# Kernel optimization log

Measured on AMD Instinct MI355X. Metric: run time of the kernel, lower is better.

Reference implementation:

```python
import jax, jax.numpy as jnp
import numpy as np

B, T, D = 1024, 256, 3
H, K, A = 128, 4, 2


def _xavier(key, shape):
    # xavier_uniform over the last two dims (per-expert [H, fan_in])
    fan_out, fan_in = shape[-2], shape[-1]
    lim = float(np.sqrt(6.0 / (fan_in + fan_out)))
    return jax.random.uniform(key, shape, minval=-lim, maxval=lim, dtype=jnp.float32)


def setup_inputs() -> dict:
    key = jax.random.key(0)
    ks = jax.random.split(key, 9)
    x = jax.random.uniform(ks[0], (B, T, D), dtype=jnp.float32)
    inp = {
        'x': x,
        'Wxr': _xavier(ks[1], (K, H, D)),
        'Wxz': _xavier(ks[2], (K, H, D)),
        'Wxn': _xavier(ks[3], (K, H, D)),
        'Whr': _xavier(ks[4], (K, H, H)),
        'Whz': _xavier(ks[5], (K, H, H)),
        'Whn': _xavier(ks[6], (K, H, H)),
        'bxr': jnp.zeros((K, H), jnp.float32),
        'bxz': jnp.zeros((K, H), jnp.float32),
        'bxn': jnp.zeros((K, H), jnp.float32),
        'brh': jnp.zeros((K, H), jnp.float32),
        'bzh': jnp.zeros((K, H), jnp.float32),
        'bnh': jnp.zeros((K, H), jnp.float32),
        'Wout': jax.random.normal(ks[7], (A, H), dtype=jnp.float32) / np.sqrt(H),
        'bout': jnp.zeros((A,), jnp.float32),
    }
    return inp


def _selector(x_t):
    # modes: 0:(a=1,r=0) 1:(a=2,r=0) 2:(a=1,r=1) 3:(a=2,r=1)
    a = jnp.argmax(x_t[:, :2], axis=-1)
    r = (x_t[:, 2] > 0.5).astype(jnp.int32)
    return jax.nn.one_hot(a + 2 * r, K, dtype=x_t.dtype)  # (B, K)


def reference(x, Wxr, Wxz, Wxn, Whr, Whz, Whn,
              bxr, bxz, bxn, brh, bzh, bnh, Wout, bout):
    def step(h, x_t):
        u = _selector(x_t)  # (B, K) one-hot
        # mixing is linear, so mix(W) @ v == mix(W @ v): compute per-expert
        # gate pre-activations then select/mix with u (avoids B*H*H temp).
        def aff_x(W, b):
            g = jnp.einsum('khd,bd->bkh', W, x_t)
            return jnp.einsum('bkh,bk->bh', g, u) + u @ b
        def aff_h(W, b):
            g = jnp.einsum('kij,bj->bki', W, h)
            return jnp.einsum('bki,bk->bi', g, u) + u @ b
        r_t = jax.nn.sigmoid(aff_x(Wxr, bxr) + aff_h(Whr, brh))
        z_t = jax.nn.sigmoid(aff_x(Wxz, bxz) + aff_h(Whz, bzh))
        n_t = jnp.tanh(aff_x(Wxn, bxn) + r_t * aff_h(Whn, bnh))
        h_new = (1.0 - z_t) * n_t + z_t * h
        logits_t = h_new @ Wout.T + bout  # (B, A)
        return h_new, logits_t

    h0 = jnp.zeros((x.shape[0], H), x.dtype)
    hT, logits_tbA = jax.lax.scan(step, h0, jnp.swapaxes(x, 0, 1))
    return jnp.swapaxes(logits_tbA, 0, 1), hT  # (B, T, A), (B, H)
```

## Files before the change

kernel.cpp:

```cpp
#include <hip/hip_runtime.h>

#define Bn 1024
#define Tn 256

typedef __attribute__((ext_vector_type(4))) float f32x4;
typedef __attribute__((ext_vector_type(2))) float f32x2;
typedef __attribute__((ext_vector_type(8))) short short8;

static __device__ __forceinline__ unsigned pack_bf16_2(float lo, float hi) {
    unsigned ul = __float_as_uint(lo), uh = __float_as_uint(hi);
    ul = (ul + 0x7fffu + ((ul >> 16) & 1u)) >> 16;
    uh = (uh + 0x7fffu + ((uh >> 16) & 1u)) >> 16;
    return (ul & 0xffffu) | (uh << 16);
}

static __device__ __forceinline__ unsigned short f2bf(float f) {
    unsigned u = __float_as_uint(f);
    return (unsigned short)((u + 0x7fffu + ((u >> 16) & 1u)) >> 16);
}

__launch_bounds__(512, 2)
__global__ void bandit_rnn(const float* __restrict__ x,
                           const float* __restrict__ Wxr, const float* __restrict__ Wxz, const float* __restrict__ Wxn,
                           const float* __restrict__ Whr, const float* __restrict__ Whz, const float* __restrict__ Whn,
                           const float* __restrict__ bxr, const float* __restrict__ bxz, const float* __restrict__ bxn,
                           const float* __restrict__ brh, const float* __restrict__ bzh, const float* __restrict__ bnh,
                           const float* __restrict__ Wout, const float* __restrict__ bout,
                           float* __restrict__ out) {
    __shared__ f32x4 comb0[512], comb1[512], comb2[512];
    __shared__ float combB[512];
    __shared__ __align__(16) unsigned short h16[2][4][136];
    __shared__ float WoutL[256];
    __shared__ float xs[2][4][3];
    __shared__ unsigned modesArr[Tn];
    __shared__ __align__(16) float spbuf[2][8][4][2];

    const int tid = threadIdx.x;
    const int w = tid >> 6;
    const int lane = tid & 63;
    const int r16 = lane & 15, q = lane >> 4;
    const int cb = blockIdx.x * 4;

    for (int p = tid; p < 2 * 4 * 136; p += 512) ((unsigned short*)h16)[p] = 0;
    {
        int p = tid;
        int k = p >> 7, i = p & 127;
        const float* wr = Wxr + (k * 128 + i) * 3;
        const float* wz = Wxz + (k * 128 + i) * 3;
        const float* wn = Wxn + (k * 128 + i) * 3;
        comb0[p] = (f32x4){wr[0], wr[1], wr[2], bxr[p] + brh[p]};
        comb1[p] = (f32x4){wz[0], wz[1], wz[2], bxz[p] + bzh[p]};
        comb2[p] = (f32x4){wn[0], wn[1], wn[2], bxn[p]};
        combB[p] = bnh[p];
    }
    if (tid < 256) WoutL[tid] = Wout[tid];
    const float b0 = bout[0], b1 = bout[1];

    if (tid < Tn) {
        const float* xp = x + (size_t)cb * (Tn * 3) + tid * 3;
        unsigned mword = 0;
#pragma unroll
        for (int c = 0; c < 4; ++c) {
            float x0 = xp[c * Tn * 3 + 0];
            float x1 = xp[c * Tn * 3 + 1];
            float x2 = xp[c * Tn * 3 + 2];
            unsigned mode = ((x1 > x0) ? 1u : 0u) + ((x2 > 0.5f) ? 2u : 0u);
            mword |= mode << (8 * c);
        }
        modesArr[tid] = mword;
    }
    if (tid < 12) {
        int c = tid / 3, j = tid % 3;
        xs[0][c][j] = x[(size_t)(cb + c) * (Tn * 3) + j];
    }

    short8 Afr[3][4][4];
    {
        const float* Wh[3] = {Whr, Whz, Whn};
#pragma unroll
        for (int g = 0; g < 3; ++g)
#pragma unroll
        for (int e = 0; e < 4; ++e)
#pragma unroll
        for (int kt = 0; kt < 4; ++kt) {
            const float* p = Wh[g] + (((e * 128) + (16 * w + r16)) * 128 + 32 * kt + 8 * q);
            float4 a0 = *(const float4*)p;
            float4 a1 = *(const float4*)(p + 4);
            union { short8 s; unsigned u[4]; } fr;
            fr.u[0] = pack_bf16_2(a0.x, a0.y);
            fr.u[1] = pack_bf16_2(a0.z, a0.w);
            fr.u[2] = pack_bf16_2(a1.x, a1.y);
            fr.u[3] = pack_bf16_2(a1.z, a1.w);
            Afr[g][e][kt] = fr.s;
        }
    }

    const int cc = r16 & 3;
    const bool jb0 = ((r16 >> 2) & 1) != 0;
    const bool jb1 = ((r16 >> 2) & 2) != 0;
    const int row = 16 * w + 4 * q + (r16 >> 2);
    float hpv = 0.f;
    __syncthreads();

#pragma unroll 1
    for (int t = 0; t < Tn; ++t) {
        const int tb = t & 1;
        if (t > 0 && tid < 8) {
            int c = tid >> 1, a = tid & 1;
            float s = a ? b1 : b0;
#pragma unroll
            for (int wv = 0; wv < 8; ++wv) s += spbuf[tb ^ 1][wv][c][a];
            out[((size_t)(cb + c) * Tn + (t - 1)) * 2 + a] = s;
        }
        float xpre = 0.f; int xc = 0, xj = 0;
        if (t + 1 < Tn && tid < 12) {
            xc = tid / 3; xj = tid % 3;
            xpre = x[(size_t)(cb + xc) * (Tn * 3) + (t + 1) * 3 + xj];
        }

        const unsigned m = modesArr[t];
        const unsigned pres = (1u << (m & 3)) | (1u << ((m >> 8) & 3)) |
                              (1u << ((m >> 16) & 3)) | (1u << ((m >> 24) & 3));
        const int mode_c = (m >> (8 * cc)) & 3;

        short8 Bf[4];
#pragma unroll
        for (int kt = 0; kt < 4; ++kt)
            Bf[kt] = *(const short8*)&h16[tb][cc][32 * kt + 8 * q];

        float selR = 0.f, selZ = 0.f, selN = 0.f;
#pragma unroll
        for (int e = 0; e < 4; ++e) {
            if (!(pres & (1u << e))) continue;
            f32x4 aR = (f32x4){0.f, 0.f, 0.f, 0.f};
            f32x4 aZ = (f32x4){0.f, 0.f, 0.f, 0.f};
            f32x4 aN = (f32x4){0.f, 0.f, 0.f, 0.f};
#pragma unroll
            for (int kt = 0; kt < 4; ++kt) {
                aR = __builtin_amdgcn_mfma_f32_16x16x32_bf16(Afr[0][e][kt], Bf[kt], aR, 0, 0, 0);
                aZ = __builtin_amdgcn_mfma_f32_16x16x32_bf16(Afr[1][e][kt], Bf[kt], aZ, 0, 0, 0);
                aN = __builtin_amdgcn_mfma_f32_16x16x32_bf16(Afr[2][e][kt], Bf[kt], aN, 0, 0, 0);
            }
            float vR = jb1 ? (jb0 ? aR[3] : aR[2]) : (jb0 ? aR[1] : aR[0]);
            float vZ = jb1 ? (jb0 ? aZ[3] : aZ[2]) : (jb0 ? aZ[1] : aZ[0]);
            float vN = jb1 ? (jb0 ? aN[3] : aN[2]) : (jb0 ? aN[1] : aN[0]);
            bool mym = (mode_c == e);
            selR = mym ? vR : selR;
            selZ = mym ? vZ : selZ;
            selN = mym ? vN : selN;
        }
        if (t + 1 < Tn && tid < 12) xs[tb ^ 1][xc][xj] = xpre;

        {
            const int kk = mode_c;
            float x0 = xs[tb][cc][0], x1 = xs[tb][cc][1], x2 = xs[tb][cc][2];
            f32x4 c0 = comb0[kk * 128 + row];
            f32x4 c1 = comb1[kk * 128 + row];
            f32x4 c2 = comb2[kk * 128 + row];
            float bn = combB[kk * 128 + row];
            float rp = selR + c0[3] + c0[0] * x0 + c0[1] * x1 + c0[2] * x2;
            float zp = selZ + c1[3] + c1[0] * x0 + c1[1] * x1 + c1[2] * x2;
            float xn =        c2[3] + c2[0] * x0 + c2[1] * x1 + c2[2] * x2;
            float r = 1.f / (1.f + __expf(-rp));
            float z = 1.f / (1.f + __expf(-zp));
            float npv = xn + r * (selN + bn);
            float ex = __expf(2.f * npv);
            float n = 1.f - 2.f / (ex + 1.f);
            float h = n + z * (hpv - n);
            hpv = h;
            h16[tb ^ 1][cc][row] = f2bf(h);
            float s0 = h * WoutL[row];
            float s1 = h * WoutL[128 + row];
            s0 += __shfl_xor(s0, 4);  s1 += __shfl_xor(s1, 4);
            s0 += __shfl_xor(s0, 8);  s1 += __shfl_xor(s1, 8);
            s0 += __shfl_xor(s0, 16); s1 += __shfl_xor(s1, 16);
            s0 += __shfl_xor(s0, 32); s1 += __shfl_xor(s1, 32);
            if (lane < 4) *(f32x2*)&spbuf[tb][w][lane][0] = (f32x2){s0, s1};
        }
        __syncthreads();
    }

    if (tid < 8) {
        int c = tid >> 1, a = tid & 1;
        float s = a ? b1 : b0;
#pragma unroll
        for (int wv = 0; wv < 8; ++wv) s += spbuf[1][wv][c][a];
        out[((size_t)(cb + c) * Tn + (Tn - 1)) * 2 + a] = s;
    }
    out[(size_t)Bn * Tn * 2 + (size_t)(cb + cc) * 128 + row] = hpv;
}

extern "C" void kernel_launch(void* const* d_in, const int* in_sizes, int n_in,
                              void* d_out, int out_size, void* d_ws, size_t ws_size,
                              hipStream_t stream) {
    const float* xin = (const float*)d_in[0];
    const float* Wxr = (const float*)d_in[1];
    const float* Wxz = (const float*)d_in[2];
    const float* Wxn = (const float*)d_in[3];
    const float* Whr = (const float*)d_in[4];
    const float* Whz = (const float*)d_in[5];
    const float* Whn = (const float*)d_in[6];
    const float* bxr = (const float*)d_in[7];
    const float* bxz = (const float*)d_in[8];
    const float* bxn = (const float*)d_in[9];
    const float* brh = (const float*)d_in[10];
    const float* bzh = (const float*)d_in[11];
    const float* bnh = (const float*)d_in[12];
    const float* Wout = (const float*)d_in[13];
    const float* bout = (const float*)d_in[14];
    float* outp = (float*)d_out;

    hipLaunchKernelGGL(bandit_rnn, dim3(256), dim3(512), 0, stream,
                       xin, Wxr, Wxz, Wxn, Whr, Whz, Whn,
                       bxr, bxz, bxn, brh, bzh, bnh, Wout, bout, outp);
}
```

Measured before the change: 350.8 us.

## Fold input projection, biases and output head into bf16 MFMA ops

Moves the per-step input affine (Wx·x plus biases) into an extra MFMA per gate by packing x and a constant one into an extra K-slice, dropping the shared-memory comb tables and scalar FMAs. The output logits are now computed by wave 0 with MFMAs over the bf16 hidden state instead of per-wave shuffle reductions and a shared partial-sum buffer. This removes LDS traffic and shuffle chains from the serial timestep loop, but adds four MFMAs per present expert and rounds x, biases and Wout to bf16, which lowers accuracy. Logits are also computed from the bf16-rounded h rather than the fp32 h.

```diff
diff --git a/kernel.cpp b/kernel.cpp
--- a/kernel.cpp
+++ b/kernel.cpp
@@ -27,34 +27,18 @@
                            const float* __restrict__ brh, const float* __restrict__ bzh, const float* __restrict__ bnh,
                            const float* __restrict__ Wout, const float* __restrict__ bout,
                            float* __restrict__ out) {
-    __shared__ f32x4 comb0[512], comb1[512], comb2[512];
-    __shared__ float combB[512];
-    __shared__ __align__(16) unsigned short h16[2][4][136];
-    __shared__ float WoutL[256];
+    __shared__ __align__(16) unsigned short h16[2][4][144];
     __shared__ float xs[2][4][3];
     __shared__ unsigned modesArr[Tn];
-    __shared__ __align__(16) float spbuf[2][8][4][2];
 
     const int tid = threadIdx.x;
     const int w = tid >> 6;
     const int lane = tid & 63;
     const int r16 = lane & 15, q = lane >> 4;
     const int cb = blockIdx.x * 4;
-
-    for (int p = tid; p < 2 * 4 * 136; p += 512) ((unsigned short*)h16)[p] = 0;
-    {
-        int p = tid;
-        int k = p >> 7, i = p & 127;
-        const float* wr = Wxr + (k * 128 + i) * 3;
-        const float* wz = Wxz + (k * 128 + i) * 3;
-        const float* wn = Wxn + (k * 128 + i) * 3;
-        comb0[p] = (f32x4){wr[0], wr[1], wr[2], bxr[p] + brh[p]};
-        comb1[p] = (f32x4){wz[0], wz[1], wz[2], bxz[p] + bzh[p]};
-        comb2[p] = (f32x4){wn[0], wn[1], wn[2], bxn[p]};
-        combB[p] = bnh[p];
-    }
-    if (tid < 256) WoutL[tid] = Wout[tid];
-    const float b0 = bout[0], b1 = bout[1];
+    const int grow = 16 * w + r16;
+
+    for (int p = tid; p < 2 * 4 * 144; p += 512) ((unsigned short*)h16)[p] = 0;
 
     if (tid < Tn) {
         const float* xp = x + (size_t)cb * (Tn * 3) + tid * 3;
@@ -83,7 +67,7 @@
         for (int e = 0; e < 4; ++e)
 #pragma unroll
         for (int kt = 0; kt < 4; ++kt) {
-            const float* p = Wh[g] + (((e * 128) + (16 * w + r16)) * 128 + 32 * kt + 8 * q);
+            const float* p = Wh[g] + (((e * 128) + grow) * 128 + 32 * kt + 8 * q);
             float4 a0 = *(const float4*)p;
             float4 a1 = *(const float4*)(p + 4);
             union { short8 s; unsigned u[4]; } fr;
@@ -94,24 +78,59 @@
             Afr[g][e][kt] = fr.s;
         }
     }
+    short8 A4r[4], A4z[4], A4n[4], A4x[4];
+#pragma unroll
+    for (int e = 0; e < 4; ++e) {
+        union { short8 s; unsigned u[4]; } fr, fz, fn, fx;
+        fr.u[0] = fr.u[1] = fr.u[2] = fr.u[3] = 0;
+        fz = fr; fn = fr; fx = fr;
+        if (q == 0) {
+            int idx = e * 128 + grow;
+            const float* wr = Wxr + idx * 3;
+            const float* wz = Wxz + idx * 3;
+            const float* wn = Wxn + idx * 3;
+            fr.u[0] = pack_bf16_2(wr[0], wr[1]);
+            fr.u[1] = pack_bf16_2(wr[2], bxr[idx] + brh[idx]);
+            fz.u[0] = pack_bf16_2(wz[0], wz[1]);
+            fz.u[1] = pack_bf16_2(wz[2], bxz[idx] + bzh[idx]);
+            fn.u[1] = pack_bf16_2(0.f, bnh[idx]);
+            fx.u[0] = pack_bf16_2(wn[0], wn[1]);
+            fx.u[1] = pack_bf16_2(wn[2], bxn[idx]);
+        }
+        A4r[e] = fr.s; A4z[e] = fz.s; A4n[e] = fn.s; A4x[e] = fx.s;
+    }
+    short8 Aout[5];
+#pragma unroll
+    for (int kt = 0; kt < 4; ++kt) {
+        union { short8 s; unsigned u[4]; } fr;
+        fr.u[0] = fr.u[1] = fr.u[2] = fr.u[3] = 0;
+        if (r16 < 2) {
+            const float* wp = Wout + r16 * 128 + 32 * kt + 8 * q;
+            fr.u[0] = pack_bf16_2(wp[0], wp[1]);
+            fr.u[1] = pack_bf16_2(wp[2], wp[3]);
+            fr.u[2] = pack_bf16_2(wp[4], wp[5]);
+            fr.u[3] = pack_bf16_2(wp[6], wp[7]);
+        }
+        Aout[kt] = fr.s;
+    }
+    {
+        union { short8 s; unsigned u[4]; } fr;
+        fr.u[0] = fr.u[1] = fr.u[2] = fr.u[3] = 0;
+        if (r16 < 2 && q == 0) fr.u[1] = pack_bf16_2(0.f, bout[r16]);
+        Aout[4] = fr.s;
+    }
 
     const int cc = r16 & 3;
     const bool jb0 = ((r16 >> 2) & 1) != 0;
     const bool jb1 = ((r16 >> 2) & 2) != 0;
-    const int row = 16 * w + 4 * q + (r16 >> 2);
+    const unsigned short one16 = 0x3F80;
     float hpv = 0.f;
+    const f32x4 zacc = (f32x4){0.f, 0.f, 0.f, 0.f};
     __syncthreads();
 
 #pragma unroll 1
     for (int t = 0; t < Tn; ++t) {
         const int tb = t & 1;
-        if (t > 0 && tid < 8) {
-            int c = tid >> 1, a = tid & 1;
-            float s = a ? b1 : b0;
-#pragma unroll
-            for (int wv = 0; wv < 8; ++wv) s += spbuf[tb ^ 1][wv][c][a];
-            out[((size_t)(cb + c) * Tn + (t - 1)) * 2 + a] = s;
-        }
         float xpre = 0.f; int xc = 0, xj = 0;
         if (t + 1 < Tn && tid < 12) {
             xc = tid / 3; xj = tid % 3;
@@ -127,14 +146,37 @@
 #pragma unroll
         for (int kt = 0; kt < 4; ++kt)
             Bf[kt] = *(const short8*)&h16[tb][cc][32 * kt + 8 * q];
-
-        float selR = 0.f, selZ = 0.f, selN = 0.f;
+        short8 Bf4;
+        {
+            union { short8 s; unsigned u[4]; } b4;
+            b4.u[0] = b4.u[1] = b4.u[2] = b4.u[3] = 0;
+            if (q == 0) {
+                float x0 = xs[tb][cc][0], x1 = xs[tb][cc][1], x2 = xs[tb][cc][2];
+                b4.u[0] = pack_bf16_2(x0, x1);
+                b4.u[1] = (unsigned)pack_bf16_2(x2, 0.f) | ((unsigned)one16 << 16);
+            }
+            Bf4 = b4.s;
+        }
+
+        if (w == 0) {
+            f32x4 alg = zacc;
+#pragma unroll
+            for (int kt = 0; kt < 4; ++kt)
+                alg = __builtin_amdgcn_mfma_f32_16x16x32_bf16(Aout[kt], Bf[kt], alg, 0, 0, 0);
+            alg = __builtin_amdgcn_mfma_f32_16x16x32_bf16(Aout[4], Bf4, alg, 0, 0, 0);
+            if (t > 0 && lane < 4)
+                *(f32x2*)&out[((size_t)(cb + lane) * Tn + (t - 1)) * 2] = (f32x2){alg[0], alg[1]};
+        }
+
+        float selR = 0.f, selZ = 0.f, selN = 0.f, selX = 0.f;
 #pragma unroll
         for (int e = 0; e < 4; ++e) {
             if (!(pres & (1u << e))) continue;
-            f32x4 aR = (f32x4){0.f, 0.f, 0.f, 0.f};
-            f32x4 aZ = (f32x4){0.f, 0.f, 0.f, 0.f};
-            f32x4 aN = (f32x4){0.f, 0.f, 0.f, 0.f};
+            f32x4 aR, aZ, aN, aX;
+            aR = __builtin_amdgcn_mfma_f32_16x16x32_bf16(A4r[e], Bf4, zacc, 0, 0, 0);
+            aZ = __builtin_amdgcn_mfma_f32_16x16x32_bf16(A4z[e], Bf4, zacc, 0, 0, 0);
+            aN = __builtin_amdgcn_mfma_f32_16x16x32_bf16(A4n[e], Bf4, zacc, 0, 0, 0);
+            aX = __builtin_amdgcn_mfma_f32_16x16x32_bf16(A4x[e], Bf4, zacc, 0, 0, 0);
 #pragma unroll
             for (int kt = 0; kt < 4; ++kt) {
                 aR = __builtin_amdgcn_mfma_f32_16x16x32_bf16(Afr[0][e][kt], Bf[kt], aR, 0, 0, 0);
@@ -144,50 +186,47 @@
             float vR = jb1 ? (jb0 ? aR[3] : aR[2]) : (jb0 ? aR[1] : aR[0]);
             float vZ = jb1 ? (jb0 ? aZ[3] : aZ[2]) : (jb0 ? aZ[1] : aZ[0]);
             float vN = jb1 ? (jb0 ? aN[3] : aN[2]) : (jb0 ? aN[1] : aN[0]);
+            float vX = jb1 ? (jb0 ? aX[3] : aX[2]) : (jb0 ? aX[1] : aX[0]);
             bool mym = (mode_c == e);
             selR = mym ? vR : selR;
             selZ = mym ? vZ : selZ;
             selN = mym ? vN : selN;
+            selX = mym ? vX : selX;
         }
         if (t + 1 < Tn && tid < 12) xs[tb ^ 1][xc][xj] = xpre;
 
         {
-            const int kk = mode_c;
-            float x0 = xs[tb][cc][0], x1 = xs[tb][cc][1], x2 = xs[tb][cc][2];
-            f32x4 c0 = comb0[kk * 128 + row];
-            f32x4 c1 = comb1[kk * 128 + row];
-            f32x4 c2 = comb2[kk * 128 + row];
-            float bn = combB[kk * 128 + row];
-            float rp = selR + c0[3] + c0[0] * x0 + c0[1] * x1 + c0[2] * x2;
-            float zp = selZ + c1[3] + c1[0] * x0 + c1[1] * x1 + c1[2] * x2;
-            float xn =        c2[3] + c2[0] * x0 + c2[1] * x1 + c2[2] * x2;
-            float r = 1.f / (1.f + __expf(-rp));
-            float z = 1.f / (1.f + __expf(-zp));
-            float npv = xn + r * (selN + bn);
+            float r = 1.f / (1.f + __expf(-selR));
+            float z = 1.f / (1.f + __expf(-selZ));
+            float npv = selX + r * selN;
             float ex = __expf(2.f * npv);
             float n = 1.f - 2.f / (ex + 1.f);
             float h = n + z * (hpv - n);
             hpv = h;
-            h16[tb ^ 1][cc][row] = f2bf(h);
-            float s0 = h * WoutL[row];
-            float s1 = h * WoutL[128 + row];
-            s0 += __shfl_xor(s0, 4);  s1 += __shfl_xor(s1, 4);
-            s0 += __shfl_xor(s0, 8);  s1 += __shfl_xor(s1, 8);
-            s0 += __shfl_xor(s0, 16); s1 += __shfl_xor(s1, 16);
-            s0 += __shfl_xor(s0, 32); s1 += __shfl_xor(s1, 32);
-            if (lane < 4) *(f32x2*)&spbuf[tb][w][lane][0] = (f32x2){s0, s1};
+            h16[tb ^ 1][cc][16 * w + 4 * q + (r16 >> 2)] = f2bf(h);
         }
         __syncthreads();
     }
 
-    if (tid < 8) {
-        int c = tid >> 1, a = tid & 1;
-        float s = a ? b1 : b0;
-#pragma unroll
-        for (int wv = 0; wv < 8; ++wv) s += spbuf[1][wv][c][a];
-        out[((size_t)(cb + c) * Tn + (Tn - 1)) * 2 + a] = s;
-    }
-    out[(size_t)Bn * Tn * 2 + (size_t)(cb + cc) * 128 + row] = hpv;
+    if (w == 0) {
+        f32x4 alg = zacc;
+#pragma unroll
+        for (int kt = 0; kt < 4; ++kt) {
+            short8 bfe = *(const short8*)&h16[Tn & 1][cc][32 * kt + 8 * q];
+            alg = __builtin_amdgcn_mfma_f32_16x16x32_bf16(Aout[kt], bfe, alg, 0, 0, 0);
+        }
+        short8 b4e;
+        {
+            union { short8 s; unsigned u[4]; } b4;
+            b4.u[0] = b4.u[1] = b4.u[2] = b4.u[3] = 0;
+            if (q == 0) b4.u[1] = ((unsigned)one16 << 16);
+            b4e = b4.s;
+        }
+        alg = __builtin_amdgcn_mfma_f32_16x16x32_bf16(Aout[4], b4e, alg, 0, 0, 0);
+        if (lane < 4)
+            *(f32x2*)&out[((size_t)(cb + lane) * Tn + (Tn - 1)) * 2] = (f32x2){alg[0], alg[1]};
+    }
+    out[(size_t)Bn * Tn * 2 + (size_t)(cb + cc) * 128 + 16 * w + 4 * q + (r16 >> 2)] = hpv;
 }
 
 extern "C" void kernel_launch(void* const* d_in, const int* in_sizes, int n_in,
```

Result: slower. 1.145 ms (+226.4%).

## Compute output logits via MFMA on wave 0, pad LDS arrays, use fast reciprocal

Applied to the files above, without the earlier changes.

The per-step output projection moves off the shuffle-reduction path. Before, every wave did xor-shuffle reductions into a shared scratch buffer that a few threads summed. Now wave 0 computes the logits for the previous step with four bf16 MFMAs, using Wout held in registers and the h fragments it already loaded. The change also pads the LDS arrays to avoid bank conflicts, replaces divisions with hardware rcp, and unrolls the time loop by two. The logits now come from bf16-rounded h rather than fp32 h, which reduces precision, and wave 0 carries extra MFMA work on the critical path.

```diff
diff --git a/kernel.cpp b/kernel.cpp
--- a/kernel.cpp
+++ b/kernel.cpp
@@ -27,33 +27,32 @@
                            const float* __restrict__ brh, const float* __restrict__ bzh, const float* __restrict__ bnh,
                            const float* __restrict__ Wout, const float* __restrict__ bout,
                            float* __restrict__ out) {
-    __shared__ f32x4 comb0[512], comb1[512], comb2[512];
-    __shared__ float combB[512];
-    __shared__ __align__(16) unsigned short h16[2][4][136];
-    __shared__ float WoutL[256];
+    __shared__ f32x4 comb0[516], comb1[516], comb2[516];
+    __shared__ float combB[516];
+    __shared__ __align__(16) unsigned short h16[2][4][144];
     __shared__ float xs[2][4][3];
     __shared__ unsigned modesArr[Tn];
-    __shared__ __align__(16) float spbuf[2][8][4][2];
 
     const int tid = threadIdx.x;
     const int w = tid >> 6;
     const int lane = tid & 63;
     const int r16 = lane & 15, q = lane >> 4;
     const int cb = blockIdx.x * 4;
-
-    for (int p = tid; p < 2 * 4 * 136; p += 512) ((unsigned short*)h16)[p] = 0;
+    const int grow = 16 * w + r16;
+
+    for (int p = tid; p < 2 * 4 * 144; p += 512) ((unsigned short*)h16)[p] = 0;
     {
         int p = tid;
         int k = p >> 7, i = p & 127;
+        int d = k * 129 + i;
         const float* wr = Wxr + (k * 128 + i) * 3;
         const float* wz = Wxz + (k * 128 + i) * 3;
         const float* wn = Wxn + (k * 128 + i) * 3;
-        comb0[p] = (f32x4){wr[0], wr[1], wr[2], bxr[p] + brh[p]};
-        comb1[p] = (f32x4){wz[0], wz[1], wz[2], bxz[p] + bzh[p]};
-        comb2[p] = (f32x4){wn[0], wn[1], wn[2], bxn[p]};
-        combB[p] = bnh[p];
-    }
-    if (tid < 256) WoutL[tid] = Wout[tid];
+        comb0[d] = (f32x4){wr[0], wr[1], wr[2], bxr[p] + brh[p]};
+        comb1[d] = (f32x4){wz[0], wz[1], wz[2], bxz[p] + bzh[p]};
+        comb2[d] = (f32x4){wn[0], wn[1], wn[2], bxn[p]};
+        combB[d] = bnh[p];
+    }
     const float b0 = bout[0], b1 = bout[1];
 
     if (tid < Tn) {
@@ -83,7 +82,7 @@
         for (int e = 0; e < 4; ++e)
 #pragma unroll
         for (int kt = 0; kt < 4; ++kt) {
-            const float* p = Wh[g] + (((e * 128) + (16 * w + r16)) * 128 + 32 * kt + 8 * q);
+            const float* p = Wh[g] + (((e * 128) + grow) * 128 + 32 * kt + 8 * q);
             float4 a0 = *(const float4*)p;
             float4 a1 = *(const float4*)(p + 4);
             union { short8 s; unsigned u[4]; } fr;
@@ -94,24 +93,32 @@
             Afr[g][e][kt] = fr.s;
         }
     }
+    short8 Aout[4];
+#pragma unroll
+    for (int kt = 0; kt < 4; ++kt) {
+        union { short8 s; unsigned u[4]; } fr;
+        fr.u[0] = fr.u[1] = fr.u[2] = fr.u[3] = 0;
+        if (r16 < 2) {
+            const float* wp = Wout + r16 * 128 + 32 * kt + 8 * q;
+            fr.u[0] = pack_bf16_2(wp[0], wp[1]);
+            fr.u[1] = pack_bf16_2(wp[2], wp[3]);
+            fr.u[2] = pack_bf16_2(wp[4], wp[5]);
+            fr.u[3] = pack_bf16_2(wp[6], wp[7]);
+        }
+        Aout[kt] = fr.s;
+    }
 
     const int cc = r16 & 3;
     const bool jb0 = ((r16 >> 2) & 1) != 0;
     const bool jb1 = ((r16 >> 2) & 2) != 0;
     const int row = 16 * w + 4 * q + (r16 >> 2);
     float hpv = 0.f;
+    const f32x4 zacc = (f32x4){0.f, 0.f, 0.f, 0.f};
     __syncthreads();
 
-#pragma unroll 1
+#pragma unroll 2
     for (int t = 0; t < Tn; ++t) {
         const int tb = t & 1;
-        if (t > 0 && tid < 8) {
-            int c = tid >> 1, a = tid & 1;
-            float s = a ? b1 : b0;
-#pragma unroll
-            for (int wv = 0; wv < 8; ++wv) s += spbuf[tb ^ 1][wv][c][a];
-            out[((size_t)(cb + c) * Tn + (t - 1)) * 2 + a] = s;
-        }
         float xpre = 0.f; int xc = 0, xj = 0;
         if (t + 1 < Tn && tid < 12) {
             xc = tid / 3; xj = tid % 3;
@@ -128,13 +135,21 @@
         for (int kt = 0; kt < 4; ++kt)
             Bf[kt] = *(const short8*)&h16[tb][cc][32 * kt + 8 * q];
 
+        if (w == 0) {
+            f32x4 alg = zacc;
+#pragma unroll
+            for (int kt = 0; kt < 4; ++kt)
+                alg = __builtin_amdgcn_mfma_f32_16x16x32_bf16(Aout[kt], Bf[kt], alg, 0, 0, 0);
+            if (t > 0 && lane < 4)
+                *(f32x2*)&out[((size_t)(cb + lane) * Tn + (t - 1)) * 2] =
+                    (f32x2){alg[0] + b0, alg[1] + b1};
+        }
+
         float selR = 0.f, selZ = 0.f, selN = 0.f;
 #pragma unroll
         for (int e = 0; e < 4; ++e) {
             if (!(pres & (1u << e))) continue;
-            f32x4 aR = (f32x4){0.f, 0.f, 0.f, 0.f};
-            f32x4 aZ = (f32x4){0.f, 0.f, 0.f, 0.f};
-            f32x4 aN = (f32x4){0.f, 0.f, 0.f, 0.f};
+            f32x4 aR = zacc, aZ = zacc, aN = zacc;
 #pragma unroll
             for (int kt = 0; kt < 4; ++kt) {
                 aR = __builtin_amdgcn_mfma_f32_16x16x32_bf16(Afr[0][e][kt], Bf[kt], aR, 0, 0, 0);
@@ -153,39 +168,37 @@
 
         {
             const int kk = mode_c;
+            const int d = kk * 129 + row;
             float x0 = xs[tb][cc][0], x1 = xs[tb][cc][1], x2 = xs[tb][cc][2];
-            f32x4 c0 = comb0[kk * 128 + row];
-            f32x4 c1 = comb1[kk * 128 + row];
-            f32x4 c2 = comb2[kk * 128 + row];
-            float bn = combB[kk * 128 + row];
+            f32x4 c0 = comb0[d];
+            f32x4 c1 = comb1[d];
+            f32x4 c2 = comb2[d];
+            float bn = combB[d];
             float rp = selR + c0[3] + c0[0] * x0 + c0[1] * x1 + c0[2] * x2;
             float zp = selZ + c1[3] + c1[0] * x0 + c1[1] * x1 + c1[2] * x2;
             float xn =        c2[3] + c2[0] * x0 + c2[1] * x1 + c2[2] * x2;
-            float r = 1.f / (1.f + __expf(-rp));
-            float z = 1.f / (1.f + __expf(-zp));
+            float r = __builtin_amdgcn_rcpf(1.f + __expf(-rp));
+            float z = __builtin_amdgcn_rcpf(1.f + __expf(-zp));
             float npv = xn + r * (selN + bn);
             float ex = __expf(2.f * npv);
-            float n = 1.f - 2.f / (ex + 1.f);
+            float n = 1.f - 2.f * __builtin_amdgcn_rcpf(ex + 1.f);
             float h = n + z * (hpv - n);
             hpv = h;
             h16[tb ^ 1][cc][row] = f2bf(h);
-            float s0 = h * WoutL[row];
-            float s1 = h * WoutL[128 + row];
-            s0 += __shfl_xor(s0, 4);  s1 += __shfl_xor(s1, 4);
-            s0 += __shfl_xor(s0, 8);  s1 += __shfl_xor(s1, 8);
-            s0 += __shfl_xor(s0, 16); s1 += __shfl_xor(s1, 16);
-            s0 += __shfl_xor(s0, 32); s1 += __shfl_xor(s1, 32);
-            if (lane < 4) *(f32x2*)&spbuf[tb][w][lane][0] = (f32x2){s0, s1};
         }
         __syncthreads();
     }
 
-    if (tid < 8) {
-        int c = tid >> 1, a = tid & 1;
-        float s = a ? b1 : b0;
-#pragma unroll
-        for (int wv = 0; wv < 8; ++wv) s += spbuf[1][wv][c][a];
-        out[((size_t)(cb + c) * Tn + (Tn - 1)) * 2 + a] = s;
+    if (w == 0) {
+        f32x4 alg = zacc;
+#pragma unroll
+        for (int kt = 0; kt < 4; ++kt) {
+            short8 bfe = *(const short8*)&h16[Tn & 1][cc][32 * kt + 8 * q];
+            alg = __builtin_amdgcn_mfma_f32_16x16x32_bf16(Aout[kt], bfe, alg, 0, 0, 0);
+        }
+        if (lane < 4)
+            *(f32x2*)&out[((size_t)(cb + lane) * Tn + (Tn - 1)) * 2] =
+                (f32x2){alg[0] + b0, alg[1] + b1};
     }
     out[(size_t)Bn * Tn * 2 + (size_t)(cb + cc) * 128 + row] = hpv;
 }
```

Measured after the change: 329.9 us. -6.0%, faster.
